# Performance work log

Hardware: AMD Instinct MI355X
Metric: run time of the kernel (lower is better)

## Reference

```python
import jax, jax.numpy as jnp
import numpy as np

B, N, T, D_MODEL, HEADS, FE = 8, 307, 48, 64, 4, 4
HD = D_MODEL // HEADS
SAMPLE_K = min(T, 5 * int(np.ceil(np.log(T))))  # = 20; also n_top u
EPS = 1e-5


def _pos_encoding(t, d):
    pos = np.arange(t, dtype=np.float32)[:, None]
    div = np.exp(np.arange(0, d, 2, dtype=np.float32) * (-np.log(10000.0) / d))
    pe = np.zeros((t, d), np.float32)
    pe[:, 0::2] = np.sin(pos * div)
    pe[:, 1::2] = np.cos(pos * div)
    return jnp.asarray(pe)


def _ln(x, g, b):
    m = x.mean(-1, keepdims=True)
    v = ((x - m) ** 2).mean(-1, keepdims=True)
    return (x - m) / jnp.sqrt(v + EPS) * g + b


def setup_inputs():
    k = jax.random.split(jax.random.key(0), 16)
    d = D_MODEL
    s = 1.0 / np.sqrt(d)
    return {
        "x": jax.random.normal(k[0], (B, N, T, d), jnp.float32),
        "time_features": jax.random.randint(k[1], (B, T, 5), 0, 10),
        "index_sample": jax.random.randint(k[2], (T, SAMPLE_K), 0, T),
        "Wq": jax.random.normal(k[3], (d, d), jnp.float32) * s,
        "Wk": jax.random.normal(k[4], (d, d), jnp.float32) * s,
        "Wv": jax.random.normal(k[5], (d, d), jnp.float32) * s,
        "Wo": jax.random.normal(k[6], (d, d), jnp.float32) * s,
        "bo": jnp.zeros((d,), jnp.float32),
        "W1": jax.random.normal(k[7], (d, FE * d), jnp.float32) * s,
        "b1": jnp.zeros((FE * d,), jnp.float32),
        "W2": jax.random.normal(k[8], (FE * d, d), jnp.float32) * (1.0 / np.sqrt(FE * d)),
        "b2": jnp.zeros((d,), jnp.float32),
        "g1": jnp.ones((d,), jnp.float32), "be1": jnp.zeros((d,), jnp.float32),
        "g2": jnp.ones((d,), jnp.float32), "be2": jnp.zeros((d,), jnp.float32),
        "emb_min": jax.random.normal(k[9], (70, d), jnp.float32) * 0.02,
        "emb_hr": jax.random.normal(k[10], (30, d), jnp.float32) * 0.02,
        "emb_wd": jax.random.normal(k[11], (10, d), jnp.float32) * 0.02,
        "emb_mo": jax.random.normal(k[12], (40, d), jnp.float32) * 0.02,
        "emb_yr": jax.random.normal(k[13], (400, d), jnp.float32) * 0.02,
    }


def reference(x, time_features, index_sample, Wq, Wk, Wv, Wo, bo, W1, b1, W2, b2,
              g1, be1, g2, be2, emb_min, emb_hr, emb_wd, emb_mo, emb_yr):
    b_, n_, t_, d = x.shape
    # temporal position + calendar embeddings (dropout is identity in eval)
    pe = _pos_encoding(t_, d)                                   # [T,d]
    tf = time_features
    tc = (emb_min[tf[..., 0]] + emb_hr[tf[..., 1]] + emb_wd[tf[..., 2]]
          + emb_mo[tf[..., 3]] + emb_yr[tf[..., 4]])             # [B,T,d]
    enc = x + pe[None, None] + tc[:, None]                       # [B,N,T,d]

    def split_heads(y):
        return y.reshape(b_, n_, t_, HEADS, HD).transpose(0, 3, 1, 2, 4)  # [B,H,N,T,HD]

    Q = split_heads(enc @ Wq)
    K = split_heads(enc @ Wk)
    V = split_heads(enc @ Wv)

    # ProbSparse attention: the torch K_expand + fancy-index is equivalent to a direct gather of K
    K_samp = K[:, :, :, index_sample, :]                         # [B,H,N,T,Sk,HD]
    qk_s = jnp.einsum('bhntd,bhntsd->bhnts', Q, K_samp)
    M = qk_s.max(-1) - qk_s.sum(-1) / SAMPLE_K                   # sparsity measure [B,H,N,T]
    _, m_top = jax.lax.top_k(M, SAMPLE_K)                        # u = SAMPLE_K, [B,H,N,u]
    Qr = jnp.take_along_axis(Q, m_top[..., None], axis=3)        # [B,H,N,u,HD]
    scores = jnp.einsum('bhnud,bhntd->bhnut', Qr, K) * (1.0 / np.sqrt(HD))
    attn = jax.nn.softmax(scores, axis=-1)
    upd = jnp.einsum('bhnut,bhntd->bhnud', attn, V)              # [B,H,N,u,HD]

    ctx = jnp.broadcast_to(V.mean(axis=3, keepdims=True), V.shape)  # initial context = mean(V)
    bi = jnp.arange(b_)[:, None, None, None]
    hi = jnp.arange(HEADS)[None, :, None, None]
    ni = jnp.arange(n_)[None, None, :, None]
    ctx = ctx.at[bi, hi, ni, m_top].set(upd)                     # scatter top-u rows

    ctx = ctx.transpose(0, 2, 3, 1, 4).reshape(b_, n_, t_, d)
    att_out = ctx @ Wo + bo
    h = _ln(att_out + enc, g1, be1)
    ff = jax.nn.relu(h @ W1 + b1) @ W2 + b2
    return _ln(ff + h, g2, be2)
```

## Files before the change

### kernel.cpp

```cpp
#include <hip/hip_runtime.h>

#define B_ 8
#define N_ 307
#define T_ 48
#define D_ 64
#define H_ 4
#define HD_ 16
#define SK_ 20
#define EPS_ 1e-5f

typedef __attribute__((ext_vector_type(8))) short bf16x8;
typedef __attribute__((ext_vector_type(4))) float f32x4;

__device__ inline ushort f2bf(float f) {
  union { float f; uint u; } x;
  x.f = f;
  uint u = x.u;
  return (ushort)((u + 0x7fffu + ((u >> 16) & 1u)) >> 16);
}
__device__ inline float bflo(uint w) { return __uint_as_float(w << 16); }
__device__ inline float bfhi(uint w) {
  return __uint_as_float(w & 0xffff0000u);
}

__global__ void prep_kernel(const int* __restrict__ tf,
                            const float* __restrict__ em,
                            const float* __restrict__ eh,
                            const float* __restrict__ ew,
                            const float* __restrict__ emo,
                            const float* __restrict__ ey,
                            float* __restrict__ tcpe,
                            const float* __restrict__ Wo,
                            const float* __restrict__ W1,
                            const float* __restrict__ W2,
                            ushort* __restrict__ WoB, ushort* __restrict__ W1B,
                            ushort* __restrict__ W2B) {
  if (blockIdx.x < 96) {
    int idx = blockIdx.x * 256 + threadIdx.x;
    if (idx >= B_ * T_ * D_) return;
    int d = idx & (D_ - 1);
    int bt = idx >> 6;
    int t = bt % T_;
    float freq = expf((float)((d >> 1) << 1) * (-logf(10000.0f) / (float)D_));
    float ang = (float)t * freq;
    float pe = (d & 1) ? cosf(ang) : sinf(ang);
    const int* f = tf + bt * 5;
    tcpe[idx] = pe + em[f[0] * D_ + d] + eh[f[1] * D_ + d] +
                ew[f[2] * D_ + d] + emo[f[3] * D_ + d] + ey[f[4] * D_ + d];
  } else {
    int idx = (blockIdx.x - 96) * 256 + threadIdx.x;
    if (idx >= 4096 + 16384 + 16384) return;
    const float* W;
    ushort* O;
    int NT, N;
    if (idx < 4096) {
      W = Wo; O = WoB; NT = 4; N = 64;
    } else if (idx < 4096 + 16384) {
      idx -= 4096; W = W1; O = W1B; NT = 16; N = 256;
    } else {
      idx -= 20480; W = W2; O = W2B; NT = 4; N = 64;
    }
    int e = idx & 7;
    int l = (idx >> 3) & 63;
    int f = idx >> 9;
    int no = f % NT, ko = f / NT;
    int k = ko * 32 + (l >> 4) * 8 + e;
    int n = no * 16 + (l & 15);
    O[idx] = f2bf(W[k * N + n]);
  }
}

__global__ __launch_bounds__(256, 4) void mega_kernel(
    const float* __restrict__ x, const int* __restrict__ idxs,
    const float* __restrict__ Wq, const float* __restrict__ Wk,
    const float* __restrict__ Wv, const ushort* __restrict__ WoB,
    const ushort* __restrict__ W1B, const ushort* __restrict__ W2B,
    const float* __restrict__ bo, const float* __restrict__ b1,
    const float* __restrict__ b2, const float* __restrict__ g1,
    const float* __restrict__ be1, const float* __restrict__ g2,
    const float* __restrict__ be2, const float* __restrict__ tcpe,
    uint* __restrict__ Vg, float* __restrict__ out) {
  __shared__ char smem[38400];
  __shared__ float s_M[H_ * T_];
  __shared__ float s_rden[H_ * SK_];
  __shared__ int s_mtop[H_ * SK_];
  float* s_enc = (float*)smem;
  float* s_k = (float*)(smem + 13056);
  float* s_q = (float*)(smem + 26112);
  ushort* ap = (ushort*)(smem + 13056);
  ushort* hs = (ushort*)(smem + 13056);

  const int tid = threadIdx.x;
  const int l = tid & 63;
  const int g = tid >> 6;
  const int bn = blockIdx.x;
  const int b = bn / N_;

  {
    const float4* x4 = (const float4*)(x + (size_t)bn * (T_ * D_));
    const float4* t4 = (const float4*)(tcpe + (size_t)b * (T_ * D_));
#pragma unroll
    for (int r = 0; r < 3; ++r) {
      int i = tid + 256 * r;
      float4 xv = x4[i];
      float4 tv = t4[i];
      int t = i >> 4;
      int d = (i & 15) << 2;
      *(float4*)&s_enc[t * 68 + d] =
          make_float4(xv.x + tv.x, xv.y + tv.y, xv.z + tv.z, xv.w + tv.w);
    }
  }
  __syncthreads();

  {
    float accq[12], acck[12], accv[12];
#pragma unroll
    for (int i = 0; i < 12; ++i) accq[i] = acck[i] = accv[i] = 0.0f;
#pragma unroll 1
    for (int kc = 0; kc < 4; ++kc) {
      float wq[16], wk[16], wv[16];
#pragma unroll
      for (int i = 0; i < 16; ++i) {
        int k = kc * 16 + i;
        wq[i] = Wq[k * D_ + l];
        wk[i] = Wk[k * D_ + l];
        wv[i] = Wv[k * D_ + l];
      }
#pragma unroll
      for (int tt = 0; tt < 12; ++tt) {
        const float* row = &s_enc[(g * 12 + tt) * 68 + kc * 16];
        float4 r0 = ((const float4*)row)[0];
        float4 r1 = ((const float4*)row)[1];
        float4 r2 = ((const float4*)row)[2];
        float4 r3 = ((const float4*)row)[3];
        float rr[16] = {r0.x, r0.y, r0.z, r0.w, r1.x, r1.y, r1.z, r1.w,
                        r2.x, r2.y, r2.z, r2.w, r3.x, r3.y, r3.z, r3.w};
#pragma unroll
        for (int i = 0; i < 16; ++i) {
          accq[tt] = fmaf(rr[i], wq[i], accq[tt]);
          acck[tt] = fmaf(rr[i], wk[i], acck[tt]);
          accv[tt] = fmaf(rr[i], wv[i], accv[tt]);
        }
      }
    }
#pragma unroll
    for (int tt = 0; tt < 12; ++tt) {
      int t = g * 12 + tt;
      s_q[t * 64 + l] = accq[tt];
      s_k[t * 68 + l] = acck[tt];
    }
    uint* vp = Vg + (size_t)bn * 1536 + g * 6 * 64 + l;
#pragma unroll
    for (int i = 0; i < 6; ++i)
      vp[i * 64] =
          (uint)f2bf(accv[2 * i]) | ((uint)f2bf(accv[2 * i + 1]) << 16);
  }
  __syncthreads();

  if (l < T_) {
    float q[16];
#pragma unroll
    for (int j = 0; j < 16; j += 4) {
      float4 v4 = *(const float4*)&s_q[l * 64 + g * HD_ + j];
      q[j] = v4.x; q[j + 1] = v4.y; q[j + 2] = v4.z; q[j + 3] = v4.w;
    }
    float mx = -1e30f, sm = 0.0f;
    for (int s = 0; s < SK_; ++s) {
      int kt = idxs[l * SK_ + s];
      float acc = 0.0f;
#pragma unroll
      for (int j = 0; j < 16; j += 4) {
        float4 kv = *(const float4*)&s_k[kt * 68 + g * HD_ + j];
        acc = fmaf(kv.x, q[j], acc);
        acc = fmaf(kv.y, q[j + 1], acc);
        acc = fmaf(kv.z, q[j + 2], acc);
        acc = fmaf(kv.w, q[j + 3], acc);
      }
      mx = fmaxf(mx, acc);
      sm += acc;
    }
    s_M[g * T_ + l] = mx - sm * (1.0f / (float)SK_);
  }
  __syncthreads();

  if (l < T_) {
    float mv = s_M[g * T_ + l];
    int rank = 0;
    for (int t2 = 0; t2 < T_; ++t2) {
      float o = s_M[g * T_ + t2];
      rank += (o > mv || (o == mv && t2 < l)) ? 1 : 0;
    }
    if (rank < SK_) s_mtop[g * SK_ + rank] = l;
  }
  __syncthreads();

  {
    float kr[16];
    if (l < T_) {
#pragma unroll
      for (int j = 0; j < 16; j += 4) {
        float4 v4 = *(const float4*)&s_k[l * 68 + g * HD_ + j];
        kr[j] = v4.x; kr[j + 1] = v4.y; kr[j + 2] = v4.z; kr[j + 3] = v4.w;
      }
    } else {
#pragma unroll
      for (int j = 0; j < 16; ++j) kr[j] = 0.0f;
    }
    __syncthreads();
#pragma unroll 1
    for (int u = 0; u < SK_; ++u) {
      int qt = s_mtop[g * SK_ + u];
      const float4* qp = (const float4*)&s_q[qt * 64 + g * HD_];
      float acc = 0.0f;
#pragma unroll
      for (int j = 0; j < 4; ++j) {
        float4 qv = qp[j];
        acc = fmaf(qv.x, kr[4 * j], acc);
        acc = fmaf(qv.y, kr[4 * j + 1], acc);
        acc = fmaf(qv.z, kr[4 * j + 2], acc);
        acc = fmaf(qv.w, kr[4 * j + 3], acc);
      }
      if (l < T_) ap[(g * SK_ + u) * T_ + l] = f2bf(__expf(acc * 0.25f));
    }
  }
  if (l < SK_) {
    const uint* a32 = (const uint*)(smem + 13056) + (g * SK_ + l) * 24;
    float s0 = 0.0f, s1 = 0.0f;
#pragma unroll
    for (int tp = 0; tp < 24; ++tp) {
      uint w = a32[tp];
      s0 += bflo(w);
      s1 += bfhi(w);
    }
    s_rden[g * SK_ + l] = 1.0f / (s0 + s1);
  }

  const int u0 = l >> 4, jj = l & 15;
  float upd[5] = {0, 0, 0, 0, 0};
  float vm = 0.0f;
  {
    const uint* a32 = (const uint*)(smem + 13056) + g * SK_ * 24;
    const uint* v32 = Vg + (size_t)bn * 1536 + g * HD_ + jj;
#pragma unroll 4
    for (int tp = 0; tp < 24; ++tp) {
      uint vw = v32[tp * 64];
      float vlo = bflo(vw), vhi = bfhi(vw);
      vm += vlo + vhi;
#pragma unroll
      for (int r = 0; r < 5; ++r) {
        uint aw = a32[(u0 + 4 * r) * 24 + tp];
        upd[r] = fmaf(bflo(aw), vlo, fmaf(bfhi(aw), vhi, upd[r]));
      }
    }
    vm *= (1.0f / (float)T_);
#pragma unroll
    for (int r = 0; r < 5; ++r) upd[r] *= s_rden[g * SK_ + u0 + 4 * r];
  }
  __syncthreads();

  {
    ushort cvm = f2bf(vm);
#pragma unroll
    for (int r = 0; r < 12; ++r) {
      int i = l + 64 * r;
      int t = i >> 4;
      hs[t * 72 + g * HD_ + jj] = cvm;
    }
    hs[(48 + u0) * 72 + g * HD_ + jj] = 0;
#pragma unroll
    for (int r = 0; r < 5; ++r) {
      int row = s_mtop[g * SK_ + u0 + 4 * r];
      hs[row * 72 + g * HD_ + jj] = f2bf(upd[r]);
    }
  }
  __syncthreads();

  ushort* ft = (ushort*)(smem + 26112) + g * 1152;
  const int kg = l >> 4, c = l & 15;
  const int row0 = g * 12;
  const f32x4 z = {0.f, 0.f, 0.f, 0.f};

  f32x4 co[4];
  {
    bf16x8 a0 = *(const bf16x8*)(const void*)(hs + (row0 + c) * 72 + kg * 8);
    bf16x8 a1 =
        *(const bf16x8*)(const void*)(hs + (row0 + c) * 72 + 32 + kg * 8);
#pragma unroll
    for (int no = 0; no < 4; ++no) {
      bf16x8 b0 = *(const bf16x8*)(const void*)(WoB + (no * 64 + l) * 8);
      bf16x8 b1f = *(const bf16x8*)(const void*)(WoB + ((4 + no) * 64 + l) * 8);
      f32x4 t0 = __builtin_amdgcn_mfma_f32_16x16x32_bf16(a0, b0, z, 0, 0, 0);
      co[no] = __builtin_amdgcn_mfma_f32_16x16x32_bf16(a1, b1f, t0, 0, 0, 0);
    }
  }
  __syncthreads();

  float h[16];
  int er[4];
#pragma unroll
  for (int reg = 0; reg < 4; ++reg) {
    int cr = kg * 4 + reg;
    er[reg] = (row0 + (cr < 12 ? cr : 11)) * 68;
  }
#pragma unroll
  for (int no = 0; no < 4; ++no) {
    int col = no * 16 + c;
    float bov = bo[col];
#pragma unroll
    for (int reg = 0; reg < 4; ++reg)
      h[no * 4 + reg] = co[no][reg] + bov + s_enc[er[reg] + col];
  }
#pragma unroll
  for (int reg = 0; reg < 4; ++reg) {
    float s = h[reg] + h[4 + reg] + h[8 + reg] + h[12 + reg];
    s += __shfl_xor(s, 1); s += __shfl_xor(s, 2);
    s += __shfl_xor(s, 4); s += __shfl_xor(s, 8);
    float mean = s * (1.0f / 64.0f);
    float d0 = h[reg] - mean, d1 = h[4 + reg] - mean;
    float d2 = h[8 + reg] - mean, d3 = h[12 + reg] - mean;
    float q = d0 * d0 + d1 * d1 + d2 * d2 + d3 * d3;
    q += __shfl_xor(q, 1); q += __shfl_xor(q, 2);
    q += __shfl_xor(q, 4); q += __shfl_xor(q, 8);
    float rstd = 1.0f / sqrtf(q * (1.0f / 64.0f) + EPS_);
#pragma unroll
    for (int no = 0; no < 4; ++no) {
      int col = no * 16 + c;
      h[no * 4 + reg] = (h[no * 4 + reg] - mean) * rstd * g1[col] + be1[col];
    }
  }
#pragma unroll
  for (int no = 0; no < 4; ++no)
#pragma unroll
    for (int reg = 0; reg < 4; ++reg) {
      int cr = kg * 4 + reg;
      if (cr < 12) hs[(row0 + cr) * 72 + no * 16 + c] = f2bf(h[no * 4 + reg]);
    }
  __syncthreads();

  f32x4 o[4] = {z, z, z, z};
  {
    bf16x8 ha0 = *(const bf16x8*)(const void*)(hs + (row0 + c) * 72 + kg * 8);
    bf16x8 ha1 =
        *(const bf16x8*)(const void*)(hs + (row0 + c) * 72 + 32 + kg * 8);
#pragma unroll 1
    for (int p = 0; p < 4; ++p) {
      f32x4 f1[4];
#pragma unroll
      for (int q = 0; q < 4; ++q) {
        int no = p * 4 + q;
        bf16x8 b0 = *(const bf16x8*)(const void*)(W1B + (no * 64 + l) * 8);
        bf16x8 b1f =
            *(const bf16x8*)(const void*)(W1B + ((16 + no) * 64 + l) * 8);
        f32x4 t0 = __builtin_amdgcn_mfma_f32_16x16x32_bf16(ha0, b0, z, 0, 0, 0);
        f1[q] = __builtin_amdgcn_mfma_f32_16x16x32_bf16(ha1, b1f, t0, 0, 0, 0);
      }
#pragma unroll
      for (int q = 0; q < 4; ++q) {
        float bb = b1[(p * 4 + q) * 16 + c];
#pragma unroll
        for (int reg = 0; reg < 4; ++reg) {
          float vv = fmaxf(f1[q][reg] + bb, 0.0f);
          ft[(kg * 4 + reg) * 72 + q * 16 + c] = f2bf(vv);
        }
      }
#pragma unroll
      for (int koi = 0; koi < 2; ++koi) {
        bf16x8 fa =
            *(const bf16x8*)(const void*)(ft + c * 72 + koi * 32 + kg * 8);
#pragma unroll
        for (int no = 0; no < 4; ++no) {
          bf16x8 bf_ = *(const bf16x8*)(const void*)(
              W2B + (((p * 2 + koi) * 4 + no) * 64 + l) * 8);
          o[no] =
              __builtin_amdgcn_mfma_f32_16x16x32_bf16(fa, bf_, o[no], 0, 0, 0);
        }
      }
    }
  }

  float* bt = (float*)smem + g * 816;
  float v[16];
#pragma unroll
  for (int no = 0; no < 4; ++no) {
    float b2v = b2[no * 16 + c];
#pragma unroll
    for (int reg = 0; reg < 4; ++reg)
      v[no * 4 + reg] = o[no][reg] + b2v + h[no * 4 + reg];
  }
#pragma unroll
  for (int reg = 0; reg < 4; ++reg) {
    float s = v[reg] + v[4 + reg] + v[8 + reg] + v[12 + reg];
    s += __shfl_xor(s, 1); s += __shfl_xor(s, 2);
    s += __shfl_xor(s, 4); s += __shfl_xor(s, 8);
    float mean = s * (1.0f / 64.0f);
    float d0 = v[reg] - mean, d1 = v[4 + reg] - mean;
    float d2 = v[8 + reg] - mean, d3 = v[12 + reg] - mean;
    float q = d0 * d0 + d1 * d1 + d2 * d2 + d3 * d3;
    q += __shfl_xor(q, 1); q += __shfl_xor(q, 2);
    q += __shfl_xor(q, 4); q += __shfl_xor(q, 8);
    float rstd = 1.0f / sqrtf(q * (1.0f / 64.0f) + EPS_);
    int cr = kg * 4 + reg;
    if (cr < 12) {
#pragma unroll
      for (int no = 0; no < 4; ++no) {
        int col = no * 16 + c;
        bt[cr * 68 + col] = (v[no * 4 + reg] - mean) * rstd * g2[col] + be2[col];
      }
    }
  }
  {
    float* op = out + ((size_t)bn * T_ + row0) * D_;
#pragma unroll
    for (int rr = 0; rr < 3; ++rr) {
      int i = l + 64 * rr;
      int row = i >> 4;
      int c4 = (i & 15) << 2;
      *(float4*)&op[row * D_ + c4] = *(const float4*)&bt[row * 68 + c4];
    }
  }
}

extern "C" void kernel_launch(void* const* d_in, const int* in_sizes, int n_in,
                              void* d_out, int out_size, void* d_ws,
                              size_t ws_size, hipStream_t stream) {
  const float* x = (const float*)d_in[0];
  const int* tf = (const int*)d_in[1];
  const int* idxs = (const int*)d_in[2];
  const float* Wq = (const float*)d_in[3];
  const float* Wk = (const float*)d_in[4];
  const float* Wv = (const float*)d_in[5];
  const float* Wo = (const float*)d_in[6];
  const float* bo = (const float*)d_in[7];
  const float* W1 = (const float*)d_in[8];
  const float* b1 = (const float*)d_in[9];
  const float* W2 = (const float*)d_in[10];
  const float* b2 = (const float*)d_in[11];
  const float* g1 = (const float*)d_in[12];
  const float* be1 = (const float*)d_in[13];
  const float* g2 = (const float*)d_in[14];
  const float* be2 = (const float*)d_in[15];
  const float* em = (const float*)d_in[16];
  const float* eh = (const float*)d_in[17];
  const float* ew = (const float*)d_in[18];
  const float* emo = (const float*)d_in[19];
  const float* ey = (const float*)d_in[20];
  float* out = (float*)d_out;

  float* tcpe = (float*)d_ws;
  ushort* WoB = (ushort*)((char*)d_ws + 98304);
  ushort* W1B = WoB + 4096;
  ushort* W2B = W1B + 16384;
  uint* Vg = (uint*)((char*)d_ws + 172032);

  hipLaunchKernelGGL(prep_kernel, dim3(240), dim3(256), 0, stream, tf, em, eh,
                     ew, emo, ey, tcpe, Wo, W1, W2, WoB, W1B, W2B);
  hipLaunchKernelGGL(mega_kernel, dim3(B_ * N_), dim3(256), 0, stream, x, idxs,
                     Wq, Wk, Wv, WoB, W1B, W2B, bo, b1, b2, g1, be1, g2, be2,
                     tcpe, Vg, out);
}
```

Measured before the change: 138.9 us.

## Keep V in shared memory instead of global scratch; reload residual from global

V is now packed as bf16 pairs into shared memory, reusing the s_enc region, instead of being written to and read back from a global workspace buffer. This removes a global round trip per block. Because s_enc is overwritten, the residual x+tcpe is re-read from global into registers before the output projection. The idxs loop is also fully unrolled with int4 loads. The trade-off is extra global reads of x and tcpe, and a barrier moved to just before the V stores.

Result: no change. 136.7 us (-1.6%).

```diff
diff --git a/kernel.cpp b/kernel.cpp
--- a/kernel.cpp
+++ b/kernel.cpp
@@ -79,7 +79,7 @@
     const float* __restrict__ b2, const float* __restrict__ g1,
     const float* __restrict__ be1, const float* __restrict__ g2,
     const float* __restrict__ be2, const float* __restrict__ tcpe,
-    uint* __restrict__ Vg, float* __restrict__ out) {
+    float* __restrict__ out) {
   __shared__ char smem[38400];
   __shared__ float s_M[H_ * T_];
   __shared__ float s_rden[H_ * SK_];
@@ -87,6 +87,7 @@
   float* s_enc = (float*)smem;
   float* s_k = (float*)(smem + 13056);
   float* s_q = (float*)(smem + 26112);
+  uint* s_v = (uint*)smem;
   ushort* ap = (ushort*)(smem + 13056);
   ushort* hs = (ushort*)(smem + 13056);
 
@@ -95,6 +96,8 @@
   const int g = tid >> 6;
   const int bn = blockIdx.x;
   const int b = bn / N_;
+  const int kg = l >> 4, c = l & 15;
+  const int row0 = g * 12;
 
   {
     const float4* x4 = (const float4*)(x + (size_t)bn * (T_ * D_));
@@ -149,13 +152,13 @@
       s_q[t * 64 + l] = accq[tt];
       s_k[t * 68 + l] = acck[tt];
     }
-    uint* vp = Vg + (size_t)bn * 1536 + g * 6 * 64 + l;
+    __syncthreads();
+    uint* vl = s_v + g * 6 * 64 + l;
 #pragma unroll
     for (int i = 0; i < 6; ++i)
-      vp[i * 64] =
+      vl[i * 64] =
           (uint)f2bf(accv[2 * i]) | ((uint)f2bf(accv[2 * i + 1]) << 16);
   }
-  __syncthreads();
 
   if (l < T_) {
     float q[16];
@@ -164,20 +167,27 @@
       float4 v4 = *(const float4*)&s_q[l * 64 + g * HD_ + j];
       q[j] = v4.x; q[j + 1] = v4.y; q[j + 2] = v4.z; q[j + 3] = v4.w;
     }
+    const int4* ip = (const int4*)(idxs + l * SK_);
     float mx = -1e30f, sm = 0.0f;
-    for (int s = 0; s < SK_; ++s) {
-      int kt = idxs[l * SK_ + s];
-      float acc = 0.0f;
-#pragma unroll
-      for (int j = 0; j < 16; j += 4) {
-        float4 kv = *(const float4*)&s_k[kt * 68 + g * HD_ + j];
-        acc = fmaf(kv.x, q[j], acc);
-        acc = fmaf(kv.y, q[j + 1], acc);
-        acc = fmaf(kv.z, q[j + 2], acc);
-        acc = fmaf(kv.w, q[j + 3], acc);
-      }
-      mx = fmaxf(mx, acc);
-      sm += acc;
+#pragma unroll
+    for (int sg = 0; sg < 5; ++sg) {
+      int4 iv = ip[sg];
+      int kts[4] = {iv.x, iv.y, iv.z, iv.w};
+#pragma unroll
+      for (int si = 0; si < 4; ++si) {
+        int kt = kts[si];
+        float acc = 0.0f;
+#pragma unroll
+        for (int j = 0; j < 16; j += 4) {
+          float4 kv = *(const float4*)&s_k[kt * 68 + g * HD_ + j];
+          acc = fmaf(kv.x, q[j], acc);
+          acc = fmaf(kv.y, q[j + 1], acc);
+          acc = fmaf(kv.z, q[j + 2], acc);
+          acc = fmaf(kv.w, q[j + 3], acc);
+        }
+        mx = fmaxf(mx, acc);
+        sm += acc;
+      }
     }
     s_M[g * T_ + l] = mx - sm * (1.0f / (float)SK_);
   }
@@ -240,7 +250,7 @@
   float vm = 0.0f;
   {
     const uint* a32 = (const uint*)(smem + 13056) + g * SK_ * 24;
-    const uint* v32 = Vg + (size_t)bn * 1536 + g * HD_ + jj;
+    const uint* v32 = s_v + g * HD_ + jj;
 #pragma unroll 4
     for (int tp = 0; tp < 24; ++tp) {
       uint vw = v32[tp * 64];
@@ -258,6 +268,22 @@
   }
   __syncthreads();
 
+  float xr[16], tr[16];
+  {
+    const float* xp = x + (size_t)bn * (T_ * D_);
+    const float* tp2 = tcpe + (size_t)b * (T_ * D_);
+#pragma unroll
+    for (int reg = 0; reg < 4; ++reg) {
+      int cr = kg * 4 + reg;
+      int rowc = row0 + (cr < 12 ? cr : 11);
+#pragma unroll
+      for (int no = 0; no < 4; ++no) {
+        xr[no * 4 + reg] = xp[rowc * D_ + no * 16 + c];
+        tr[no * 4 + reg] = tp2[rowc * D_ + no * 16 + c];
+      }
+    }
+  }
+
   {
     ushort cvm = f2bf(vm);
 #pragma unroll
@@ -276,8 +302,6 @@
   __syncthreads();
 
   ushort* ft = (ushort*)(smem + 26112) + g * 1152;
-  const int kg = l >> 4, c = l & 15;
-  const int row0 = g * 12;
   const f32x4 z = {0.f, 0.f, 0.f, 0.f};
 
   f32x4 co[4];
@@ -296,19 +320,14 @@
   __syncthreads();
 
   float h[16];
-  int er[4];
-#pragma unroll
-  for (int reg = 0; reg < 4; ++reg) {
-    int cr = kg * 4 + reg;
-    er[reg] = (row0 + (cr < 12 ? cr : 11)) * 68;
-  }
 #pragma unroll
   for (int no = 0; no < 4; ++no) {
     int col = no * 16 + c;
     float bov = bo[col];
 #pragma unroll
     for (int reg = 0; reg < 4; ++reg)
-      h[no * 4 + reg] = co[no][reg] + bov + s_enc[er[reg] + col];
+      h[no * 4 + reg] =
+          co[no][reg] + bov + xr[no * 4 + reg] + tr[no * 4 + reg];
   }
 #pragma unroll
   for (int reg = 0; reg < 4; ++reg) {
@@ -450,11 +469,10 @@
   ushort* WoB = (ushort*)((char*)d_ws + 98304);
   ushort* W1B = WoB + 4096;
   ushort* W2B = W1B + 16384;
-  uint* Vg = (uint*)((char*)d_ws + 172032);
 
   hipLaunchKernelGGL(prep_kernel, dim3(240), dim3(256), 0, stream, tf, em, eh,
                      ew, emo, ey, tcpe, Wo, W1, W2, WoB, W1B, W2B);
   hipLaunchKernelGGL(mega_kernel, dim3(B_ * N_), dim3(256), 0, stream, x, idxs,
                      Wq, Wk, Wv, WoB, W1B, W2B, bo, b1, b2, g1, be1, g2, be2,
-                     tcpe, Vg, out);
+                     tcpe, out);
 }
```
